# Kernel optimization log

Measured on AMD Instinct MI355X. Metric: run time of the kernel, lower is better.

The kernel has to match this reference:

```python
import jax, jax.numpy as jnp
import numpy as np

T, B, H, N = 1024, 8, 8, 32  # x dim D = H*N*N = 8192


def setup_inputs() -> dict:
    key = jax.random.key(0)
    x = jax.random.normal(key, (T, B, H * N * N), dtype=jnp.float32)
    S = jnp.zeros((B, H, N, N), dtype=jnp.float32)
    scale = jnp.float32(1.0)  # init_scale
    bias = jnp.float32(2.0)   # init_bias
    return {"x": x, "S": S, "scale": scale, "bias": bias}


def reference(x, S, scale, bias):
    Tt, Bb, D = x.shape
    _, Hh, n, _ = S.shape
    xr = x.reshape(Tt, Bb, Hh, n, n)  # [T,B,H,n,n]

    def step(S_c, A):
        # A: [B,H,n,n]
        k = A.mean(axis=-1)            # mean over dim 2 per head -> [B,H,n]
        v = A.mean(axis=-2)            # mean over dim 1 per head -> [B,H,n]
        A_mean = A.mean(axis=(-1, -2))  # [B,H]
        beta = jax.nn.sigmoid(scale * A_mean + bias)  # [B,H]
        k_norm = k / (jnp.linalg.norm(k, axis=-1, keepdims=True) + 1e-6)
        retrieved = jnp.einsum('bhij,bhj->bhi', S_c, k_norm)
        delta = v - retrieved
        outer = delta[..., :, None] * k_norm[..., None, :]  # [B,H,n,n]
        S_new = jnp.tanh(beta[..., None, None] * S_c + outer)
        Sq = jnp.einsum('bhij,bhj->bhi', S_new, k_norm)     # [B,H,n]
        out = Sq * jax.nn.silu(Sq)                          # [B,H,n]
        return S_new, out.reshape(Bb, Hh * n)

    S_final, output = jax.lax.scan(step, S, xr)  # output: [T,B,H*n]
    return output, S_final
```

## Files before the change

### kernel.cpp

```cpp
#include <hip/hip_runtime.h>
#include <math.h>

#define T_STEPS 1024
#define NBH     64
#define NTILE   65536

static __device__ __forceinline__ float fast_rcp(float x) {
  return __builtin_amdgcn_rcpf(x);
}
static __device__ __forceinline__ float fast_sigmoid(float x) {
  return fast_rcp(1.0f + __expf(-x));
}
static __device__ __forceinline__ float fast_tanh(float x) {
  return 1.0f - 2.0f * fast_rcp(1.0f + __expf(2.0f * x));
}

template <int CTRL>
static __device__ __forceinline__ float dpp_add(float x) {
  int y = __builtin_amdgcn_update_dpp(0, __float_as_int(x), CTRL, 0xF, 0xF, true);
  return x + __int_as_float(y);
}

static __device__ __forceinline__ float red16(float x) {
  x = dpp_add<0xB1>(x);
  x = dpp_add<0x4E>(x);
  x = dpp_add<0x141>(x);
  x = dpp_add<0x140>(x);
  return x;
}

__global__ __launch_bounds__(256) void stats_kernel(
    const float* __restrict__ x, const float* __restrict__ scale_p,
    const float* __restrict__ bias_p, float* __restrict__ knT2,
    float* __restrict__ vvT2, float* __restrict__ bbT2) {
  const int tid = threadIdx.x;
  const int l   = tid & 63;
  const int m   = l & 7;
  const int g   = l >> 3;
  const int wid    = (blockIdx.x * blockDim.x + tid) >> 6;
  const int nwaves = (gridDim.x * blockDim.x) >> 6;
  const float sc = scale_p[0], bi = bias_p[0];

  for (int tile = wid; tile < NTILE; tile += nwaves) {
    const int t  = tile >> 6;
    const int bh = tile & 63;
    const float4* xp = (const float4*)(x + (size_t)tile * 1024);
    const float4 a0 = xp[l];
    const float4 a1 = xp[l + 64];
    const float4 a2 = xp[l + 128];
    const float4 a3 = xp[l + 192];

    float r0 = (a0.x + a0.y) + (a0.z + a0.w);
    float r1 = (a1.x + a1.y) + (a1.z + a1.w);
    float r2 = (a2.x + a2.y) + (a2.z + a2.w);
    float r3 = (a3.x + a3.y) + (a3.z + a3.w);
    r0 += __shfl_xor(r0, 1); r1 += __shfl_xor(r1, 1);
    r2 += __shfl_xor(r2, 1); r3 += __shfl_xor(r3, 1);
    r0 += __shfl_xor(r0, 2); r1 += __shfl_xor(r1, 2);
    r2 += __shfl_xor(r2, 2); r3 += __shfl_xor(r3, 2);
    r0 += __shfl_xor(r0, 4); r1 += __shfl_xor(r1, 4);
    r2 += __shfl_xor(r2, 4); r3 += __shfl_xor(r3, 4);

    float c0 = a0.x + a1.x + a2.x + a3.x;
    float c1 = a0.y + a1.y + a2.y + a3.y;
    float c2 = a0.z + a1.z + a2.z + a3.z;
    float c3 = a0.w + a1.w + a2.w + a3.w;
    c0 += __shfl_xor(c0, 8);  c1 += __shfl_xor(c1, 8);
    c2 += __shfl_xor(c2, 8);  c3 += __shfl_xor(c3, 8);
    c0 += __shfl_xor(c0, 16); c1 += __shfl_xor(c1, 16);
    c2 += __shfl_xor(c2, 16); c3 += __shfl_xor(c3, 16);
    c0 += __shfl_xor(c0, 32); c1 += __shfl_xor(c1, 32);
    c2 += __shfl_xor(c2, 32); c3 += __shfl_xor(c3, 32);

    float t1 = (r0 + r1) + (r2 + r3);
    float t2 = (r0 * r0 + r1 * r1) + (r2 * r2 + r3 * r3);
    t1 += __shfl_xor(t1, 8);  t2 += __shfl_xor(t2, 8);
    t1 += __shfl_xor(t1, 16); t2 += __shfl_xor(t2, 16);
    t1 += __shfl_xor(t1, 32); t2 += __shfl_xor(t2, 32);
    const float norm = sqrtf(t2) * (1.0f / 32.0f);
    const float ks   = (1.0f / 32.0f) * fast_rcp(norm + 1e-6f);

    const size_t base = (size_t)bh * 32 * T_STEPS + t;
    if (m == 0) {
      knT2[base + (size_t)(g)      * T_STEPS] = r0 * ks;
      knT2[base + (size_t)(g + 8)  * T_STEPS] = r1 * ks;
      knT2[base + (size_t)(g + 16) * T_STEPS] = r2 * ks;
      knT2[base + (size_t)(g + 24) * T_STEPS] = r3 * ks;
    }
    if (l < 8) {
      vvT2[base + (size_t)(4 * m)     * T_STEPS] = c0 * (1.0f / 32.0f);
      vvT2[base + (size_t)(4 * m + 1) * T_STEPS] = c1 * (1.0f / 32.0f);
      vvT2[base + (size_t)(4 * m + 2) * T_STEPS] = c2 * (1.0f / 32.0f);
      vvT2[base + (size_t)(4 * m + 3) * T_STEPS] = c3 * (1.0f / 32.0f);
    }
    if (l == 0) {
      const float mean = t1 * (1.0f / 1024.0f);
      bbT2[(size_t)bh * T_STEPS + t] = fast_sigmoid(sc * mean + bi);
    }
  }
}

__global__ __launch_bounds__(256, 1) void scan_kernel(
    const float* __restrict__ S0, const float* __restrict__ knT2,
    const float* __restrict__ vvT2, const float* __restrict__ bbT2,
    float* __restrict__ out, float* __restrict__ Sfin) {
  const int tid  = threadIdx.x;
  const int lane = tid & 63;
  const int g    = lane >> 4;
  const int s    = lane & 15;
  const int w    = blockIdx.x * 4 + (tid >> 6);
  const int bh   = w >> 3;
  const int i    = (w & 7) * 4 + g;
  const int chain = bh * 32 + i;

  const float2 sini = *(const float2*)(S0 + (size_t)bh * 1024 + i * 32 + 2 * s);
  float Sa = sini.x, Sb = sini.y;

  const float* kn0p = knT2 + ((size_t)bh * 32 + 2 * s) * T_STEPS;
  const float* kn1p = kn0p + T_STEPS;
  const float* vp   = vvT2 + ((size_t)bh * 32 + i) * T_STEPS;
  const float* bp   = bbT2 + (size_t)bh * T_STEPS;

  float Ak0[16], Ak1[16], Av[16], Ab[16];
  float Bk0[16], Bk1[16], Bv[16], Bb[16];

#define LOAD_BLK(K0, K1, VV, BE, TOFF)                                    \
  do {                                                                    \
    const int _to = (TOFF);                                               \
    _Pragma("unroll")                                                     \
    for (int qq = 0; qq < 4; ++qq) {                                      \
      *(float4*)&K0[4 * qq] = *(const float4*)(kn0p + _to + 4 * qq);      \
      *(float4*)&K1[4 * qq] = *(const float4*)(kn1p + _to + 4 * qq);      \
      *(float4*)&VV[4 * qq] = *(const float4*)(vp   + _to + 4 * qq);      \
      *(float4*)&BE[4 * qq] = *(const float4*)(bp   + _to + 4 * qq);      \
    }                                                                     \
  } while (0)

#define STEP_BLK(K0, K1, VV, BE, TBASE)                                   \
  do {                                                                    \
    float oacc = 0.0f;                                                    \
    _Pragma("unroll")                                                     \
    for (int u = 0; u < 16; ++u) {                                        \
      const float c0 = K0[u], c1 = K1[u];                                 \
      float r = red16(Sa * c0 + Sb * c1);                                 \
      const float d  = VV[u] - r;                                         \
      const float bc = BE[u];                                             \
      Sa = fast_tanh(bc * Sa + d * c0);                                   \
      Sb = fast_tanh(bc * Sb + d * c1);                                   \
      float qv = red16(Sa * c0 + Sb * c1);                                \
      const float o = qv * qv * fast_sigmoid(qv);                         \
      oacc = (u == s) ? o : oacc;                                         \
    }                                                                     \
    outp[(size_t)((TBASE) + s) * 2048] = oacc;                            \
  } while (0)

  float* outp = out + chain;

  LOAD_BLK(Ak0, Ak1, Av, Ab, 0);

  for (int t0 = 0; t0 < T_STEPS; t0 += 32) {
    const int tB = t0 + 16;
    const int tA2 = (t0 + 32 < T_STEPS) ? t0 + 32 : t0;
    LOAD_BLK(Bk0, Bk1, Bv, Bb, tB);
    STEP_BLK(Ak0, Ak1, Av, Ab, t0);
    LOAD_BLK(Ak0, Ak1, Av, Ab, tA2);
    STEP_BLK(Bk0, Bk1, Bv, Bb, tB);
  }

#undef LOAD_BLK
#undef STEP_BLK

  float2 sfin; sfin.x = Sa; sfin.y = Sb;
  *(float2*)(Sfin + (size_t)bh * 1024 + i * 32 + 2 * s) = sfin;
}

extern "C" void kernel_launch(void* const* d_in, const int* in_sizes, int n_in,
                              void* d_out, int out_size, void* d_ws, size_t ws_size,
                              hipStream_t stream) {
  const float* x     = (const float*)d_in[0];
  const float* S0    = (const float*)d_in[1];
  const float* scale = (const float*)d_in[2];
  const float* bias  = (const float*)d_in[3];
  float* out = (float*)d_out;

  float* knT2 = (float*)d_ws;
  float* vvT2 = knT2 + (size_t)NTILE * 32;
  float* bbT2 = vvT2 + (size_t)NTILE * 32;

  stats_kernel<<<2048, 256, 0, stream>>>(x, scale, bias, knT2, vvT2, bbT2);

  float* Sfin = out + (size_t)T_STEPS * 2048;
  scan_kernel<<<128, 256, 0, stream>>>(S0, knT2, vvT2, bbT2, out, Sfin);
}
```

Baseline: 493.7 us.

## Stage per-wave stats in LDS for coalesced stores and fold tanh scaling

The stats kernel now gives each wave a fixed (bh, 16-timestep) job. It prefetches the next x tile while reducing the current one, buffers k/v/beta results in shared memory, and writes them out as coalesced float4 rows instead of scattered strided scalar stores. The factor of 2 from tanh(2x) is folded into the stored v and beta values, so the scan's inner loop saves a multiply per element (D2 = 2v - 2r). This cuts uncoalesced global writes and a little latency-bound scan arithmetic, at the cost of extra LDS use and fewer parallel waves in the stats launch.

```diff
diff --git a/kernel.cpp b/kernel.cpp
--- a/kernel.cpp
+++ b/kernel.cpp
@@ -11,8 +11,8 @@
 static __device__ __forceinline__ float fast_sigmoid(float x) {
   return fast_rcp(1.0f + __expf(-x));
 }
-static __device__ __forceinline__ float fast_tanh(float x) {
-  return 1.0f - 2.0f * fast_rcp(1.0f + __expf(2.0f * x));
+static __device__ __forceinline__ float fast_tanh2(float y) {
+  return 1.0f - 2.0f * fast_rcp(1.0f + __expf(y));
 }
 
 template <int CTRL>
@@ -37,18 +37,28 @@
   const int l   = tid & 63;
   const int m   = l & 7;
   const int g   = l >> 3;
-  const int wid    = (blockIdx.x * blockDim.x + tid) >> 6;
-  const int nwaves = (gridDim.x * blockDim.x) >> 6;
+  const int wib = tid >> 6;
+  const int job = blockIdx.x * 4 + wib;
+  const int bh  = job >> 6;
+  const int t0  = (job & 63) << 4;
   const float sc = scale_p[0], bi = bias_p[0];
 
-  for (int tile = wid; tile < NTILE; tile += nwaves) {
-    const int t  = tile >> 6;
-    const int bh = tile & 63;
-    const float4* xp = (const float4*)(x + (size_t)tile * 1024);
-    const float4 a0 = xp[l];
-    const float4 a1 = xp[l + 64];
-    const float4 a2 = xp[l + 128];
-    const float4 a3 = xp[l + 192];
+  __shared__ float kn_s[4][512];
+  __shared__ float vv_s[4][512];
+  __shared__ float bb_s[4][16];
+  float* ks = kn_s[wib];
+  float* vs = vv_s[wib];
+  float* bs = bb_s[wib];
+
+  const float4* xp = (const float4*)(x + ((size_t)t0 * 64 + bh) * 1024);
+  float4 a0 = xp[l], a1 = xp[l + 64], a2 = xp[l + 128], a3 = xp[l + 192];
+
+  for (int tt = 0; tt < 16; ++tt) {
+    float4 b0, b1, b2, b3;
+    if (tt < 15) {
+      const float4* xn = xp + (size_t)(tt + 1) * 16384;
+      b0 = xn[l]; b1 = xn[l + 64]; b2 = xn[l + 128]; b3 = xn[l + 192];
+    }
 
     float r0 = (a0.x + a0.y) + (a0.z + a0.w);
     float r1 = (a1.x + a1.y) + (a1.z + a1.w);
@@ -78,25 +88,42 @@
     t1 += __shfl_xor(t1, 16); t2 += __shfl_xor(t2, 16);
     t1 += __shfl_xor(t1, 32); t2 += __shfl_xor(t2, 32);
     const float norm = sqrtf(t2) * (1.0f / 32.0f);
-    const float ks   = (1.0f / 32.0f) * fast_rcp(norm + 1e-6f);
-
-    const size_t base = (size_t)bh * 32 * T_STEPS + t;
+    const float kscl = (1.0f / 32.0f) * fast_rcp(norm + 1e-6f);
+
     if (m == 0) {
-      knT2[base + (size_t)(g)      * T_STEPS] = r0 * ks;
-      knT2[base + (size_t)(g + 8)  * T_STEPS] = r1 * ks;
-      knT2[base + (size_t)(g + 16) * T_STEPS] = r2 * ks;
-      knT2[base + (size_t)(g + 24) * T_STEPS] = r3 * ks;
+      ks[(g)      * 16 + tt] = r0 * kscl;
+      ks[(g + 8)  * 16 + tt] = r1 * kscl;
+      ks[(g + 16) * 16 + tt] = r2 * kscl;
+      ks[(g + 24) * 16 + tt] = r3 * kscl;
     }
     if (l < 8) {
-      vvT2[base + (size_t)(4 * m)     * T_STEPS] = c0 * (1.0f / 32.0f);
-      vvT2[base + (size_t)(4 * m + 1) * T_STEPS] = c1 * (1.0f / 32.0f);
-      vvT2[base + (size_t)(4 * m + 2) * T_STEPS] = c2 * (1.0f / 32.0f);
-      vvT2[base + (size_t)(4 * m + 3) * T_STEPS] = c3 * (1.0f / 32.0f);
+      vs[(4 * m)     * 16 + tt] = c0 * (1.0f / 16.0f);
+      vs[(4 * m + 1) * 16 + tt] = c1 * (1.0f / 16.0f);
+      vs[(4 * m + 2) * 16 + tt] = c2 * (1.0f / 16.0f);
+      vs[(4 * m + 3) * 16 + tt] = c3 * (1.0f / 16.0f);
     }
     if (l == 0) {
       const float mean = t1 * (1.0f / 1024.0f);
-      bbT2[(size_t)bh * T_STEPS + t] = fast_sigmoid(sc * mean + bi);
-    }
+      bs[tt] = 2.0f * fast_sigmoid(sc * mean + bi);
+    }
+
+    a0 = b0; a1 = b1; a2 = b2; a3 = b3;
+  }
+
+  const size_t rowbase = (size_t)bh * 32 * T_STEPS + t0;
+#pragma unroll
+  for (int rep = 0; rep < 2; ++rep) {
+    const int c = l + rep * 64;
+    const int e = c >> 2;
+    const int q = c & 3;
+    const float4 kv = *(const float4*)&ks[e * 16 + q * 4];
+    const float4 vv = *(const float4*)&vs[e * 16 + q * 4];
+    *(float4*)(knT2 + rowbase + (size_t)e * T_STEPS + q * 4) = kv;
+    *(float4*)(vvT2 + rowbase + (size_t)e * T_STEPS + q * 4) = vv;
+  }
+  if (l < 4) {
+    const float4 bv = *(const float4*)&bs[l * 4];
+    *(float4*)(bbT2 + (size_t)bh * T_STEPS + t0 + l * 4) = bv;
   }
 }
 
@@ -142,13 +169,13 @@
     _Pragma("unroll")                                                     \
     for (int u = 0; u < 16; ++u) {                                        \
       const float c0 = K0[u], c1 = K1[u];                                 \
-      float r = red16(Sa * c0 + Sb * c1);                                 \
-      const float d  = VV[u] - r;                                         \
-      const float bc = BE[u];                                             \
-      Sa = fast_tanh(bc * Sa + d * c0);                                   \
-      Sb = fast_tanh(bc * Sb + d * c1);                                   \
-      float qv = red16(Sa * c0 + Sb * c1);                                \
-      const float o = qv * qv * fast_sigmoid(qv);                         \
+      const float r  = red16(Sa * c0 + Sb * c1);                          \
+      const float D2 = fmaf(-2.0f, r, VV[u]);              \
+      const float B2 = BE[u];                                             \
+      Sa = fast_tanh2(fmaf(B2, Sa, D2 * c0));                             \
+      Sb = fast_tanh2(fmaf(B2, Sb, D2 * c1));                             \
+      const float qv = red16(Sa * c0 + Sb * c1);                          \
+      const float o  = qv * qv * fast_sigmoid(qv);                        \
       oacc = (u == s) ? o : oacc;                                         \
     }                                                                     \
     outp[(size_t)((TBASE) + s) * 2048] = oacc;                            \
@@ -187,7 +214,7 @@
   float* vvT2 = knT2 + (size_t)NTILE * 32;
   float* bbT2 = vvT2 + (size_t)NTILE * 32;
 
-  stats_kernel<<<2048, 256, 0, stream>>>(x, scale, bias, knT2, vvT2, bbT2);
+  stats_kernel<<<1024, 256, 0, stream>>>(x, scale, bias, knT2, vvT2, bbT2);
 
   float* Sfin = out + (size_t)T_STEPS * 2048;
   scan_kernel<<<128, 256, 0, stream>>>(S0, knT2, vvT2, bbT2, out, Sfin);
```

Result: faster. 465.8 us (-5.7%).
